# Kernel optimization log

Hardware: AMD Instinct MI355X
Metric: run time of the kernel (lower is better)

## Reference

```python
import jax, jax.numpy as jnp
import numpy as np

# Window-batch of 16x16 windows from a U-Net stage
B, C, H, W = 128, 128, 16, 16
HEADS = 8
EQK, EV = 128, 512      # embed_dim_qk, embed_dim_v (embed_dim=512, ratio=4)
L = H * W               # tokens per window (stride=1)


def _conv3x3(x, w, b):
    # NCHW 3x3 conv, padding 1
    out = jax.lax.conv_general_dilated(x, w, (1, 1), ((1, 1), (1, 1)),
                                       dimension_numbers=('NCHW', 'OIHW', 'NCHW'))
    return out + b[None, :, None, None]


def _pos_att(q, wq, bq, wk, bk, wv, bv, wo, bo, gamma):
    # MultiHeadAttention2D_POS, stride=1 -> conv_q/k/v are 1x1 convs
    hd, hdv = EQK // HEADS, EV // HEADS

    def proj(x, w, bias, d):
        y = jnp.einsum('bchw,ec->behw', x, w) + bias[None, :, None, None]
        return y.reshape(B, HEADS, d, L).transpose(0, 1, 3, 2)  # (B,h,L,d)

    pq = proj(q, wq, bq, hd)
    pk = proj(q, wk, bk, hd)
    pv = proj(q, wv, bv, hdv)
    attn = jax.nn.softmax(jnp.einsum('bhqd,bhkd->bhqk', pq, pk) * hd ** -0.5, axis=-1)
    out = jnp.einsum('bhqk,bhkd->bhqd', attn, pv)
    out = out.transpose(0, 1, 3, 2).reshape(B, EV, H, W)
    out = _conv3x3(out, wo, bo)             # proj_out: 3x3 conv EV->C
    return q + out * gamma                  # gamma-scaled residual


def _cha_att(q, wq, bq, wk, bk, wv, bv, wo, bo, gamma):
    # MultiHeadAttention2D_CHA: depthwise 1x1 grouped convs (channel multiplier = HEADS),
    # attention over the CHANNEL axis. Faithfully reproduces torch's reshape of the
    # group-major (c*HEADS+h) channel layout into (B, heads, C, L).
    def dwproj(x, w, bias):
        y = (x[:, :, None] * w.reshape(C, HEADS)[None, :, :, None, None]
             + bias.reshape(C, HEADS)[None, :, :, None, None])
        return y.reshape(B, C * HEADS, H, W).reshape(B, HEADS, C, L)

    pq = dwproj(q, wq, bq)
    pk = dwproj(q, wk, bk)
    pv = dwproj(q, wv, bv)
    attn = jax.nn.softmax(jnp.einsum('bhcl,bhdl->bhcd', pq, pk) * L ** -0.5, axis=-1)
    out = jnp.einsum('bhcd,bhdl->bhcl', attn, pv)      # (B,h,C,L)
    out = out.reshape(B, HEADS * C, H, W)
    # proj_out: grouped 1x1 ConvTranspose (== grouped 1x1 conv): sum each HEADS-sized group
    out = (out.reshape(B, C, HEADS, H, W)
           * wo.reshape(C, HEADS)[None, :, :, None, None]).sum(2) + bo[None, :, None, None]
    return q + out * gamma


def _forward(qkv_pos, qkv_cha,
             pos_wq, pos_bq, pos_wk, pos_bk, pos_wv, pos_bv, pos_wo, pos_bo, gamma_pos,
             cha_wq, cha_bq, cha_wk, cha_bk, cha_wv, cha_bv, cha_wo, cha_bo, gamma_cha,
             fuse_w, fuse_b):
    out_pos = _pos_att(qkv_pos, pos_wq, pos_bq, pos_wk, pos_bk, pos_wv, pos_bv,
                       pos_wo, pos_bo, gamma_pos)
    out_cha = _cha_att(qkv_cha, cha_wq, cha_bq, cha_wk, cha_bk, cha_wv, cha_bv,
                       cha_wo, cha_bo, gamma_cha)
    out = (out_pos + out_cha) * 0.5          # att_fusion='add' (slides=0 -> full slices)
    return _conv3x3(out, fuse_w, fuse_b)     # conv_out (Dropout2d is identity at eval)


def setup_inputs() -> dict:
    key = jax.random.key(0)
    ks = jax.random.split(key, 24)
    n = lambda k, shape, s=0.05: jax.random.normal(k, shape, dtype=jnp.float32) * s
    return {
        'qkv_pos': jax.random.normal(ks[0], (B, C, H, W), jnp.float32),
        'qkv_cha': jax.random.normal(ks[1], (B, C, H, W), jnp.float32),
        'pos_wq': n(ks[2], (EQK, C)), 'pos_bq': n(ks[3], (EQK,)),
        'pos_wk': n(ks[4], (EQK, C)), 'pos_bk': n(ks[5], (EQK,)),
        'pos_wv': n(ks[6], (EV, C)), 'pos_bv': n(ks[7], (EV,)),
        'pos_wo': n(ks[8], (C, EV, 3, 3)), 'pos_bo': n(ks[9], (C,)),
        'gamma_pos': jnp.array(0.1, jnp.float32),
        'cha_wq': n(ks[10], (C * HEADS,)), 'cha_bq': n(ks[11], (C * HEADS,)),
        'cha_wk': n(ks[12], (C * HEADS,)), 'cha_bk': n(ks[13], (C * HEADS,)),
        'cha_wv': n(ks[14], (C * HEADS,)), 'cha_bv': n(ks[15], (C * HEADS,)),
        'cha_wo': n(ks[16], (C * HEADS,)), 'cha_bo': n(ks[17], (C,)),
        'gamma_cha': jnp.array(0.1, jnp.float32),
        'fuse_w': n(ks[18], (C, C, 3, 3)), 'fuse_b': n(ks[19], (C,)),
    }


def reference(qkv_pos, qkv_cha,
              pos_wq, pos_bq, pos_wk, pos_bk, pos_wv, pos_bv, pos_wo, pos_bo, gamma_pos,
              cha_wq, cha_bq, cha_wk, cha_bk, cha_wv, cha_bv, cha_wo, cha_bo, gamma_cha,
              fuse_w, fuse_b):
    return _forward(qkv_pos, qkv_cha,
                    pos_wq, pos_bq, pos_wk, pos_bk, pos_wv, pos_bv, pos_wo, pos_bo, gamma_pos,
                    cha_wq, cha_bq, cha_wk, cha_bk, cha_wv, cha_bv, cha_wo, cha_bo, gamma_cha,
                    fuse_w, fuse_b)
```

## Files before the change

### kernel.cpp

```cpp
#include <hip/hip_runtime.h>
#include <cstdint>
#include <cstddef>

typedef unsigned short ushort_t;
typedef unsigned int uint_t;
typedef __attribute__((ext_vector_type(8))) short bf16x8;
typedef __attribute__((ext_vector_type(4))) float f32x4;

#define NB 128
#define NC 128
#define NL 256
#define NH 8
#define HD 16
#define HDV 64
#define NEV 512
#define PHALF 4194304

__device__ __forceinline__ ushort_t f2bf(float f) {
    uint_t u = __float_as_uint(f);
    u += 0x7fffu + ((u >> 16) & 1u);
    return (ushort_t)(u >> 16);
}
__device__ __forceinline__ float bf2f(ushort_t s) {
    return __uint_as_float(((uint_t)s) << 16);
}
__device__ __forceinline__ uint_t pack2(float lo, float hi) {
    uint_t r;
    asm("v_cvt_pk_bf16_f32 %0, %1, %2" : "=v"(r) : "v"(lo), "v"(hi));
    return r;
}

template<int CIN>
__global__ __launch_bounds__(256) void k_wpack(const float* __restrict__ w,
                                               short* __restrict__ wp) {
    int idx = blockIdx.x * 256 + threadIdx.x;
    if (idx >= CIN * 1152) return;
    int j    = idx & 7;
    int lane = (idx >> 3) & 63;
    int frag = idx >> 9;
    int rt   = frag & 7;
    int tap  = (frag >> 3) % 9;
    int ch   = frag / 72;
    int co   = rt * 16 + (lane & 15);
    int g    = lane >> 4;
    int ci   = ch * 32 + g * 8 + j;
    wp[idx] = (short)f2bf(w[((size_t)co * CIN + ci) * 9 + tap]);
}

template<int E>
__global__ __launch_bounds__(256) void k_wpack_qkv(const float* __restrict__ w,
                                                   short* __restrict__ wp) {
    int idx = blockIdx.x * 256 + threadIdx.x;
    if (idx >= E * 128) return;
    int j    = idx & 7;
    int lane = (idx >> 3) & 63;
    int ch   = (idx >> 9) & 3;
    int rt   = idx >> 11;
    int n = lane & 15, g = lane >> 4;
    wp[idx] = (short)f2bf(w[(size_t)(rt*16 + n)*128 + ch*32 + g*8 + j]);
}

__global__ __launch_bounds__(256) void k_xpose(const float* __restrict__ x,
                                               ushort_t* __restrict__ xbf) {
    const int half = blockIdx.x, b = blockIdx.y, t = threadIdx.x;
    const float* src = x + (size_t)b*NC*NL + (size_t)half*64*NL + t;
    uint_t* dst = (uint_t*)(xbf + ((size_t)b*NL + t)*NC + half*64);
    #pragma unroll
    for (int k8 = 0; k8 < 8; ++k8) {
        uint4 u;
        u.x = pack2(src[(k8*8+0)*NL], src[(k8*8+1)*NL]);
        u.y = pack2(src[(k8*8+2)*NL], src[(k8*8+3)*NL]);
        u.z = pack2(src[(k8*8+4)*NL], src[(k8*8+5)*NL]);
        u.w = pack2(src[(k8*8+6)*NL], src[(k8*8+7)*NL]);
        *(uint4*)(dst + k8*4) = u;
    }
}

__global__ __launch_bounds__(256) void k_pos_mfma(
    const ushort_t* __restrict__ xbf,
    const short* __restrict__ wpq, const short* __restrict__ wpk,
    const short* __restrict__ wpv,
    const float* __restrict__ bq, const float* __restrict__ bk,
    const float* __restrict__ bv,
    ushort_t* __restrict__ att)
{
    const int h = blockIdx.x, b = blockIdx.y;
    const int t = threadIdx.x;
    const int lane = t & 63, w = t >> 6;
    const int n = lane & 15, g = lane >> 4;

    __shared__ __align__(16) short lds[31744];

    const f32x4 z4 = {0.f, 0.f, 0.f, 0.f};
    f32x4 qacc[4], kacc[4], vacc[4][4];
    #pragma unroll
    for (int ct = 0; ct < 4; ++ct) { qacc[ct] = z4; kacc[ct] = z4; }
    #pragma unroll
    for (int vt = 0; vt < 4; ++vt)
        #pragma unroll
        for (int ct = 0; ct < 4; ++ct) vacc[vt][ct] = z4;

    const ushort_t* xr = xbf + ((size_t)(b*NL + w*64 + n))*NC;

    #pragma unroll 2
    for (int ch = 0; ch < 4; ++ch) {
        bf16x8 xb[4];
        #pragma unroll
        for (int ct = 0; ct < 4; ++ct)
            xb[ct] = *(const bf16x8*)(xr + ct*16*NC + ch*32 + g*8);
        const size_t fo = ((size_t)((h*4 + ch)*64) + lane) * 8;
        {
            bf16x8 aq = *(const bf16x8*)(wpq + fo);
            #pragma unroll
            for (int ct = 0; ct < 4; ++ct)
                qacc[ct] = __builtin_amdgcn_mfma_f32_16x16x32_bf16(aq, xb[ct], qacc[ct], 0, 0, 0);
        }
        {
            bf16x8 ak = *(const bf16x8*)(wpk + fo);
            #pragma unroll
            for (int ct = 0; ct < 4; ++ct)
                kacc[ct] = __builtin_amdgcn_mfma_f32_16x16x32_bf16(ak, xb[ct], kacc[ct], 0, 0, 0);
        }
        #pragma unroll
        for (int vt = 0; vt < 4; ++vt) {
            bf16x8 av = *(const bf16x8*)(wpv + ((size_t)((((h*4 + vt)*4) + ch)*64) + lane) * 8);
            #pragma unroll
            for (int ct = 0; ct < 4; ++ct)
                vacc[vt][ct] = __builtin_amdgcn_mfma_f32_16x16x32_bf16(xb[ct], av, vacc[vt][ct], 0, 0, 0);
        }
    }

    {
        float bqv[4], bkv[4];
        #pragma unroll
        for (int r = 0; r < 4; ++r) {
            bqv[r] = bq[h*16 + g*4 + r];
            bkv[r] = bk[h*16 + g*4 + r];
        }
        #pragma unroll
        for (int ct = 0; ct < 4; ++ct) {
            uint2 qp, kp;
            qp.x = pack2(qacc[ct][0] + bqv[0], qacc[ct][1] + bqv[1]);
            qp.y = pack2(qacc[ct][2] + bqv[2], qacc[ct][3] + bqv[3]);
            *(uint2*)&lds[6144 + w*1536 + (ct*16 + n)*24 + g*4] = qp;
            kp.x = pack2(kacc[ct][0] + bkv[0], kacc[ct][1] + bkv[1]);
            kp.y = pack2(kacc[ct][2] + bkv[2], kacc[ct][3] + bkv[3]);
            *(uint2*)&lds[(w*64 + ct*16 + n)*24 + g*4] = kp;
        }
        #pragma unroll
        for (int vt = 0; vt < 4; ++vt) {
            const float bvv = bv[h*64 + vt*16 + n];
            #pragma unroll
            for (int ct = 0; ct < 4; ++ct) {
                uint2 vp;
                vp.x = pack2(vacc[vt][ct][0] + bvv, vacc[vt][ct][1] + bvv);
                vp.y = pack2(vacc[vt][ct][2] + bvv, vacc[vt][ct][3] + bvv);
                *(uint2*)&lds[14848 + (vt*16 + n)*264 + w*64 + ct*16 + g*4] = vp;
            }
        }
    }
    __syncthreads();

    #pragma unroll 1
    for (int qt = 0; qt < 4; ++qt) {
        bf16x8 qf = (bf16x8){0,0,0,0,0,0,0,0};
        if (g < 2) qf = *(const bf16x8*)&lds[6144 + w*1536 + (qt*16 + n)*24 + g*8];
        f32x4 s[16];
        #pragma unroll
        for (int kt = 0; kt < 16; ++kt) {
            bf16x8 kf = (bf16x8){0,0,0,0,0,0,0,0};
            if (g < 2) kf = *(const bf16x8*)&lds[(kt*16 + n)*24 + g*8];
            s[kt] = __builtin_amdgcn_mfma_f32_16x16x32_bf16(kf, qf, z4, 0, 0, 0);
        }
        float den = 0.f;
        #pragma unroll
        for (int kt = 0; kt < 16; ++kt)
            #pragma unroll
            for (int r = 0; r < 4; ++r) {
                float e = exp2f(s[kt][r] * 0.36067376022224085f);
                s[kt][r] = e;
                den += e;
            }
        den += __shfl_xor(den, 16);
        den += __shfl_xor(den, 32);
        const float inv = 1.f / den;

        f32x4 oacc[4] = {z4, z4, z4, z4};
        #pragma unroll
        for (int c2 = 0; c2 < 8; ++c2) {
            #pragma unroll
            for (int u = 0; u < 2; ++u) {
                const int kt = 2*c2 + u;
                uint2 pp;
                pp.x = pack2(s[kt][0], s[kt][1]);
                pp.y = pack2(s[kt][2], s[kt][3]);
                *(uint2*)&lds[12288 + w*640 + n*40 + u*16 + g*4] = pp;
            }
            bf16x8 pf = *(const bf16x8*)&lds[12288 + w*640 + n*40 + g*8];
            #pragma unroll
            for (int vt = 0; vt < 4; ++vt) {
                bf16x8 av = *(const bf16x8*)&lds[14848 + (vt*16 + n)*264 + c2*32 + g*8];
                oacc[vt] = __builtin_amdgcn_mfma_f32_16x16x32_bf16(av, pf, oacc[vt], 0, 0, 0);
            }
        }
        ushort_t* ap = att + (((size_t)b*NL + (w*64 + qt*16 + n))*NEV + h*HDV + g*4);
        #pragma unroll
        for (int vt = 0; vt < 4; ++vt) {
            uint2 op;
            op.x = pack2(oacc[vt][0]*inv, oacc[vt][1]*inv);
            op.y = pack2(oacc[vt][2]*inv, oacc[vt][3]*inv);
            *(uint2*)(ap + vt*16) = op;
        }
    }
}

__global__ __launch_bounds__(512, 2) void k_conv_ci(
    const ushort_t* __restrict__ att, const short* __restrict__ wp,
    ushort_t* __restrict__ P)
{
    const int kc = blockIdx.x, b = blockIdx.y;
    const int t = threadIdx.x;
    const int lane = t & 63, w = t >> 6;
    const int wr = w >> 2, wc = w & 3;
    const int n = lane & 15, gl = lane >> 4;

    __shared__ __align__(16) short ims[2][10368];

    {
        bf16x8 z = {0,0,0,0,0,0,0,0};
        bf16x8* p = (bf16x8*)&ims[0][0];
        for (int i = t; i < 2592; i += 512) p[i] = z;
    }

    f32x4 acc[4][4];
    #pragma unroll
    for (int i = 0; i < 4; ++i)
        #pragma unroll
        for (int j = 0; j < 4; ++j) acc[i][j] = (f32x4){0.f,0.f,0.f,0.f};

    const int g1 = t & 3, x1 = (t >> 2) & 15, y1 = t >> 6;
    const ushort_t* src1 = att + ((size_t)(b*NL + y1*16 + x1))*NEV + kc*256 + g1*8;
    const ushort_t* src2 = att + ((size_t)(b*NL + (y1+8)*16 + x1))*NEV + kc*256 + g1*8;
    const int slot1 = (((y1+1)*4 + g1)*18 + x1 + 1) * 8;
    const int slot2 = (((y1+9)*4 + g1)*18 + x1 + 1) * 8;

    bf16x8 v1 = *(const bf16x8*)src1;
    bf16x8 v2 = *(const bf16x8*)src2;
    __syncthreads();

    #pragma unroll 1
    for (int ch = 0; ch < 8; ++ch) {
        short* buf = &ims[ch & 1][0];
        *(bf16x8*)&buf[slot1] = v1;
        *(bf16x8*)&buf[slot2] = v2;
        if (ch < 7) {
            v1 = *(const bf16x8*)(src1 + (ch + 1) * 32);
            v2 = *(const bf16x8*)(src2 + (ch + 1) * 32);
        }
        __syncthreads();
        #pragma unroll
        for (int tap = 0; tap < 9; ++tap) {
            const int dy = tap / 3, dx = tap % 3;
            bf16x8 Bf[4];
            #pragma unroll
            for (int ct = 0; ct < 4; ++ct)
                Bf[ct] = *(const bf16x8*)&buf[((((wc*4 + ct + dy)*4) + gl)*18 + n + dx) * 8];
            bf16x8 Af[4];
            #pragma unroll
            for (int rt = 0; rt < 4; ++rt)
                Af[rt] = *(const bf16x8*)(wp +
                    ((size_t)(((kc*8 + ch)*9 + tap)*8 + wr*4 + rt)) * 512 + lane*8);
            #pragma unroll
            for (int rt = 0; rt < 4; ++rt)
                #pragma unroll
                for (int ct = 0; ct < 4; ++ct)
                    acc[rt][ct] = __builtin_amdgcn_mfma_f32_16x16x32_bf16(
                        Af[rt], Bf[ct], acc[rt][ct], 0, 0, 0);
        }
    }

    ushort_t* Pb = P + (size_t)kc * PHALF + (size_t)b * NL * NC;
    #pragma unroll
    for (int rt = 0; rt < 4; ++rt) {
        const int co0 = wr*64 + rt*16 + gl*4;
        #pragma unroll
        for (int ct = 0; ct < 4; ++ct) {
            const int l = wc*64 + ct*16 + n;
            uint2 u;
            u.x = pack2(acc[rt][ct][0], acc[rt][ct][1]);
            u.y = pack2(acc[rt][ct][2], acc[rt][ct][3]);
            *(uint2*)(Pb + (size_t)l*NC + co0) = u;
        }
    }
}

__global__ __launch_bounds__(512, 2) void k_conv_co(
    const float* __restrict__ comb, const short* __restrict__ wp,
    const float* __restrict__ bias, float* __restrict__ out)
{
    const int kc = blockIdx.x, b = blockIdx.y;
    const int t = threadIdx.x;
    const int lane = t & 63, w = t >> 6;
    const int wr = w & 1, wc = w >> 1;
    const int n = lane & 15, gl = lane >> 4;

    __shared__ __align__(16) short ims[2][10368];

    {
        bf16x8 z = {0,0,0,0,0,0,0,0};
        bf16x8* p = (bf16x8*)&ims[0][0];
        for (int i = t; i < 2592; i += 512) p[i] = z;
    }

    f32x4 acc[2][4];
    #pragma unroll
    for (int i = 0; i < 2; ++i)
        #pragma unroll
        for (int j = 0; j < 4; ++j) acc[i][j] = (f32x4){0.f,0.f,0.f,0.f};

    const int g1 = t & 3, x1 = (t >> 2) & 15, y1 = t >> 6;
    const float* s1 = comb + ((size_t)(b*NL + y1*16 + x1))*NC + g1*8;
    const float* s2 = comb + ((size_t)(b*NL + (y1+8)*16 + x1))*NC + g1*8;
    const int slot1 = (((y1+1)*4 + g1)*18 + x1 + 1) * 8;
    const int slot2 = (((y1+9)*4 + g1)*18 + x1 + 1) * 8;

    float4 a1 = *(const float4*)s1,       b1_ = *(const float4*)(s1 + 4);
    float4 a2 = *(const float4*)s2,       b2_ = *(const float4*)(s2 + 4);
    __syncthreads();

    #pragma unroll 1
    for (int ch = 0; ch < 4; ++ch) {
        short* buf = &ims[ch & 1][0];
        uint4 w1, w2;
        w1.x = pack2(a1.x, a1.y);   w1.y = pack2(a1.z, a1.w);
        w1.z = pack2(b1_.x, b1_.y); w1.w = pack2(b1_.z, b1_.w);
        w2.x = pack2(a2.x, a2.y);   w2.y = pack2(a2.z, a2.w);
        w2.z = pack2(b2_.x, b2_.y); w2.w = pack2(b2_.z, b2_.w);
        *(uint4*)&buf[slot1] = w1;
        *(uint4*)&buf[slot2] = w2;
        if (ch < 3) {
            a1  = *(const float4*)(s1 + (ch+1)*32);
            b1_ = *(const float4*)(s1 + (ch+1)*32 + 4);
            a2  = *(const float4*)(s2 + (ch+1)*32);
            b2_ = *(const float4*)(s2 + (ch+1)*32 + 4);
        }
        __syncthreads();
        #pragma unroll
        for (int tap = 0; tap < 9; ++tap) {
            const int dy = tap / 3, dx = tap % 3;
            bf16x8 Bf[4];
            #pragma unroll
            for (int ct = 0; ct < 4; ++ct)
                Bf[ct] = *(const bf16x8*)&buf[((((wc*4 + ct + dy)*4) + gl)*18 + n + dx) * 8];
            bf16x8 Af[2];
            #pragma unroll
            for (int rt = 0; rt < 2; ++rt)
                Af[rt] = *(const bf16x8*)(wp +
                    ((size_t)((ch*9 + tap)*8 + kc*4 + wr*2 + rt)) * 512 + lane*8);
            #pragma unroll
            for (int rt = 0; rt < 2; ++rt)
                #pragma unroll
                for (int ct = 0; ct < 4; ++ct)
                    acc[rt][ct] = __builtin_amdgcn_mfma_f32_16x16x32_bf16(
                        Af[rt], Bf[ct], acc[rt][ct], 0, 0, 0);
        }
    }

    #pragma unroll
    for (int rt = 0; rt < 2; ++rt) {
        const int co0 = kc*64 + wr*32 + rt*16 + gl*4;
        const float c0 = bias[co0+0], c1 = bias[co0+1],
                    c2 = bias[co0+2], c3 = bias[co0+3];
        #pragma unroll
        for (int ct = 0; ct < 4; ++ct) {
            const int l = wc*64 + ct*16 + n;
            f32x4 a = acc[rt][ct];
            out[((size_t)b*NC + co0+0)*NL + l] = c0 + a[0];
            out[((size_t)b*NC + co0+1)*NL + l] = c1 + a[1];
            out[((size_t)b*NC + co0+2)*NL + l] = c2 + a[2];
            out[((size_t)b*NC + co0+3)*NL + l] = c3 + a[3];
        }
    }
}

#define NLP 260
__global__ __launch_bounds__(256) void k_cha(
    const float* __restrict__ xc,
    const float* __restrict__ cwq, const float* __restrict__ cbq,
    const float* __restrict__ cwk, const float* __restrict__ cbk,
    const float* __restrict__ cwv, const float* __restrict__ cbv,
    const float* __restrict__ cwo, const float* __restrict__ cbo,
    const float* __restrict__ gamma,
    const ushort_t* __restrict__ P, const float* __restrict__ qpos,
    const float* __restrict__ pbo, const float* __restrict__ gpos,
    float* __restrict__ comb)
{
    const int h = blockIdx.x, b = blockIdx.y, t = threadIdx.x;
    __shared__ float qh[16][NLP];
    __shared__ float G_s[16][17];
    __shared__ float S_s[16];
    __shared__ float wq_s[128], bq_s[128], wk_s[128], bk_s[128], wv_s[128], bv_s[128];
    __shared__ float A_s[128][17];
    __shared__ float B_s[128];
    __shared__ float M_s[16][17];
    __shared__ float c_s[16];

    #pragma unroll
    for (int j = 0; j < 16; ++j)
        qh[j][t] = xc[((size_t)b*NC + h*16 + j)*NL + t];
    if (t < 128) {
        const int k = h*128 + t;
        wq_s[t] = cwq[k]; bq_s[t] = cbq[k];
        wk_s[t] = cwk[k]; bk_s[t] = cbk[k];
        wv_s[t] = cwv[k]; bv_s[t] = cbv[k];
    }
    __syncthreads();
    {
        const int i = t >> 4, j = t & 15;
        const float4* qi = (const float4*)qh[i];
        const float4* qj = (const float4*)qh[j];
        float gg = 0.f;
        for (int l4 = 0; l4 < NL/4; ++l4) {
            float4 a = qi[l4], c = qj[l4];
            gg = fmaf(a.x,c.x,fmaf(a.y,c.y,fmaf(a.z,c.z,fmaf(a.w,c.w,gg))));
        }
        G_s[i][j] = gg;
    }
    if (t < 16) {
        const float4* qi = (const float4*)qh[t];
        float s = 0.f;
        for (int l4 = 0; l4 < NL/4; ++l4) { float4 a = qi[l4]; s += a.x + a.y + a.z + a.w; }
        S_s[t] = s;
    }
    __syncthreads();
    if (t < 128) {
        const int c2 = t, cg = c2 >> 3;
        const float wqc = wq_s[c2], bqc = bq_s[c2];
        float Pv[16];
        #pragma unroll
        for (int j = 0; j < 16; ++j) Pv[j] = wqc*G_s[cg][j] + bqc*S_s[j];
        const float Qc = wqc*S_s[cg] + bqc*256.0f;
        float mx = -3.0e38f;
        #pragma unroll
        for (int dg = 0; dg < 16; ++dg) {
            #pragma unroll
            for (int dj = 0; dj < 8; ++dj) {
                const int d = dg*8 + dj;
                float s = wk_s[d]*Pv[dg] + bk_s[d]*Qc;
                mx = fmaxf(mx, s);
            }
        }
        float A[16];
        #pragma unroll
        for (int j = 0; j < 16; ++j) A[j] = 0.f;
        float Bv = 0.f, den = 0.f;
        #pragma unroll
        for (int dg = 0; dg < 16; ++dg) {
            #pragma unroll
            for (int dj = 0; dj < 8; ++dj) {
                const int d = dg*8 + dj;
                float s = wk_s[d]*Pv[dg] + bk_s[d]*Qc;
                float e = __expf((s - mx) * 0.0625f);
                den += e;
                A[dg] = fmaf(e, wv_s[d], A[dg]);
                Bv = fmaf(e, bv_s[d], Bv);
            }
        }
        const float inv = 1.f / den;
        #pragma unroll
        for (int j = 0; j < 16; ++j) A_s[c2][j] = A[j]*inv;
        B_s[c2] = Bv*inv;
    }
    __syncthreads();
    {
        const int cl = t >> 4, j = t & 15;
        const int cp = h*16 + cl;
        float m = 0.f;
        #pragma unroll
        for (int hp = 0; hp < 8; ++hp)
            m = fmaf(cwo[cp*8+hp], A_s[cl*8+hp][j], m);
        M_s[cl][j] = m;
        if (j == 0) {
            float cc = cbo[cp];
            #pragma unroll
            for (int hp = 0; hp < 8; ++hp)
                cc = fmaf(cwo[cp*8+hp], B_s[cl*8+hp], cc);
            c_s[cl] = cc;
        }
    }
    __syncthreads();
    {
        const float g  = gamma[0];
        const float gp = gpos[0];
        const int l = t;
        float av[16];
        #pragma unroll
        for (int cl = 0; cl < 16; ++cl) {
            float a = c_s[cl];
            #pragma unroll
            for (int j = 0; j < 16; ++j)
                a = fmaf(M_s[cl][j], qh[j][l], a);
            av[cl] = a;
        }
        const ushort_t* p0 = P + ((size_t)b*NL + l)*NC + h*16;
        const ushort_t* p1 = p0 + PHALF;
        const float* qp = qpos + ((size_t)b*NC + h*16)*NL + l;
        float4* cp4 = (float4*)(comb + ((size_t)b*NL + l)*NC + h*16);
        #pragma unroll
        for (int q = 0; q < 4; ++q) {
            uint2 u0 = *(const uint2*)(p0 + 4*q);
            uint2 u1 = *(const uint2*)(p1 + 4*q);
            float s0 = bf2f((ushort_t)(u0.x & 0xffffu)) + bf2f((ushort_t)(u1.x & 0xffffu));
            float s1 = bf2f((ushort_t)(u0.x >> 16))     + bf2f((ushort_t)(u1.x >> 16));
            float s2 = bf2f((ushort_t)(u0.y & 0xffffu)) + bf2f((ushort_t)(u1.y & 0xffffu));
            float s3 = bf2f((ushort_t)(u0.y >> 16))     + bf2f((ushort_t)(u1.y >> 16));
            float4 c;
            c.x = 0.5f*(qp[(4*q+0)*NL] + gp*(pbo[h*16+4*q+0] + s0) + qh[4*q+0][l] + g*av[4*q+0]);
            c.y = 0.5f*(qp[(4*q+1)*NL] + gp*(pbo[h*16+4*q+1] + s1) + qh[4*q+1][l] + g*av[4*q+1]);
            c.z = 0.5f*(qp[(4*q+2)*NL] + gp*(pbo[h*16+4*q+2] + s2) + qh[4*q+2][l] + g*av[4*q+2]);
            c.w = 0.5f*(qp[(4*q+3)*NL] + gp*(pbo[h*16+4*q+3] + s3) + qh[4*q+3][l] + g*av[4*q+3]);
            cp4[q] = c;
        }
    }
}

extern "C" void kernel_launch(void* const* d_in, const int* in_sizes, int n_in,
                              void* d_out, int out_size, void* d_ws, size_t ws_size,
                              hipStream_t stream)
{
    const float* qpos = (const float*)d_in[0];
    const float* qcha = (const float*)d_in[1];
    const float* pwq  = (const float*)d_in[2];
    const float* pbq  = (const float*)d_in[3];
    const float* pwk  = (const float*)d_in[4];
    const float* pbk  = (const float*)d_in[5];
    const float* pwv  = (const float*)d_in[6];
    const float* pbv  = (const float*)d_in[7];
    const float* pwo  = (const float*)d_in[8];
    const float* pbo  = (const float*)d_in[9];
    const float* gpos = (const float*)d_in[10];
    const float* cwq  = (const float*)d_in[11];
    const float* cbq  = (const float*)d_in[12];
    const float* cwk  = (const float*)d_in[13];
    const float* cbk  = (const float*)d_in[14];
    const float* cwv  = (const float*)d_in[15];
    const float* cbv  = (const float*)d_in[16];
    const float* cwo  = (const float*)d_in[17];
    const float* cbo  = (const float*)d_in[18];
    const float* gcha = (const float*)d_in[19];
    const float* fw   = (const float*)d_in[20];
    const float* fb   = (const float*)d_in[21];
    float* outp = (float*)d_out;

    char* ws = (char*)d_ws;
    ushort_t* att  = (ushort_t*)ws;
    float*    comb = (float*)ws;
    ushort_t* P    = (ushort_t*)(ws + 33554432);
    ushort_t* xbf  = (ushort_t*)(ws + 33554432);
    short*    wp1  = (short*)(ws + 50331648);
    short*    wp2  = (short*)(ws + 51511296);
    short*    wpq  = (short*)(ws + 51806208);
    short*    wpk  = (short*)(ws + 51838976);
    short*    wpv  = (short*)(ws + 51871744);

    k_wpack<NEV><<<dim3((NEV*1152 + 255)/256), 256, 0, stream>>>(pwo, wp1);
    k_wpack<NC ><<<dim3((NC *1152 + 255)/256), 256, 0, stream>>>(fw,  wp2);
    k_wpack_qkv<128><<<dim3(64),  256, 0, stream>>>(pwq, wpq);
    k_wpack_qkv<128><<<dim3(64),  256, 0, stream>>>(pwk, wpk);
    k_wpack_qkv<512><<<dim3(256), 256, 0, stream>>>(pwv, wpv);

    k_xpose<<<dim3(2, NB), 256, 0, stream>>>(qpos, xbf);
    k_pos_mfma<<<dim3(NH, NB), 256, 0, stream>>>(xbf, wpq, wpk, wpv,
                                                 pbq, pbk, pbv, att);
    k_conv_ci<<<dim3(2, NB), 512, 0, stream>>>(att, wp1, P);
    k_cha<<<dim3(NH, NB), 256, 0, stream>>>(qcha, cwq, cbq, cwk, cbk, cwv, cbv,
                                            cwo, cbo, gcha,
                                            P, qpos, pbo, gpos, comb);
    k_conv_co<<<dim3(2, NB), 512, 0, stream>>>(comb, wp2, fb, outp);
}
```

Baseline: 181.8 us.

## Shrink attention LDS via bpermute Q exchange and split conv_ci by row halves

New measurement: 181.6 us. About the same (-0.1%).

```diff
diff --git a/kernel.cpp b/kernel.cpp
--- a/kernel.cpp
+++ b/kernel.cpp
@@ -89,7 +89,7 @@
     const int lane = t & 63, w = t >> 6;
     const int n = lane & 15, g = lane >> 4;
 
-    __shared__ __align__(16) short lds[31744];
+    __shared__ __align__(16) short lds[23552];
 
     const f32x4 z4 = {0.f, 0.f, 0.f, 0.f};
     f32x4 qacc[4], kacc[4], vacc[4][4];
@@ -130,6 +130,7 @@
         }
     }
 
+    uint_t qu01[4], qu23[4];
     {
         float bqv[4], bkv[4];
         #pragma unroll
@@ -139,13 +140,12 @@
         }
         #pragma unroll
         for (int ct = 0; ct < 4; ++ct) {
-            uint2 qp, kp;
-            qp.x = pack2(qacc[ct][0] + bqv[0], qacc[ct][1] + bqv[1]);
-            qp.y = pack2(qacc[ct][2] + bqv[2], qacc[ct][3] + bqv[3]);
-            *(uint2*)&lds[6144 + w*1536 + (ct*16 + n)*24 + g*4] = qp;
+            qu01[ct] = pack2(qacc[ct][0] + bqv[0], qacc[ct][1] + bqv[1]);
+            qu23[ct] = pack2(qacc[ct][2] + bqv[2], qacc[ct][3] + bqv[3]);
+            uint2 kp;
             kp.x = pack2(kacc[ct][0] + bkv[0], kacc[ct][1] + bkv[1]);
             kp.y = pack2(kacc[ct][2] + bkv[2], kacc[ct][3] + bkv[3]);
-            *(uint2*)&lds[(w*64 + ct*16 + n)*24 + g*4] = kp;
+            *(uint2*)&lds[(w*64 + ct*16 + n)*16 + g*4] = kp;
         }
         #pragma unroll
         for (int vt = 0; vt < 4; ++vt) {
@@ -155,21 +155,28 @@
                 uint2 vp;
                 vp.x = pack2(vacc[vt][ct][0] + bvv, vacc[vt][ct][1] + bvv);
                 vp.y = pack2(vacc[vt][ct][2] + bvv, vacc[vt][ct][3] + bvv);
-                *(uint2*)&lds[14848 + (vt*16 + n)*264 + w*64 + ct*16 + g*4] = vp;
+                *(uint2*)&lds[6656 + (vt*16 + n)*264 + w*64 + ct*16 + g*4] = vp;
             }
         }
     }
     __syncthreads();
 
+    const int a0 = (n + 32*(g & 1)) * 4;
     #pragma unroll 1
     for (int qt = 0; qt < 4; ++qt) {
-        bf16x8 qf = (bf16x8){0,0,0,0,0,0,0,0};
-        if (g < 2) qf = *(const bf16x8*)&lds[6144 + w*1536 + (qt*16 + n)*24 + g*8];
+        union { uint_t u[4]; bf16x8 v; } qfu;
+        qfu.u[0] = (uint_t)__builtin_amdgcn_ds_bpermute(a0,      (int)qu01[qt]);
+        qfu.u[1] = (uint_t)__builtin_amdgcn_ds_bpermute(a0,      (int)qu23[qt]);
+        qfu.u[2] = (uint_t)__builtin_amdgcn_ds_bpermute(a0 + 64, (int)qu01[qt]);
+        qfu.u[3] = (uint_t)__builtin_amdgcn_ds_bpermute(a0 + 64, (int)qu23[qt]);
+        if (g >= 2) { qfu.u[0] = 0; qfu.u[1] = 0; qfu.u[2] = 0; qfu.u[3] = 0; }
+        bf16x8 qf = qfu.v;
+
         f32x4 s[16];
         #pragma unroll
         for (int kt = 0; kt < 16; ++kt) {
             bf16x8 kf = (bf16x8){0,0,0,0,0,0,0,0};
-            if (g < 2) kf = *(const bf16x8*)&lds[(kt*16 + n)*24 + g*8];
+            if (g < 2) kf = *(const bf16x8*)&lds[(kt*16 + n)*16 + g*8];
             s[kt] = __builtin_amdgcn_mfma_f32_16x16x32_bf16(kf, qf, z4, 0, 0, 0);
         }
         float den = 0.f;
@@ -194,12 +201,12 @@
                 uint2 pp;
                 pp.x = pack2(s[kt][0], s[kt][1]);
                 pp.y = pack2(s[kt][2], s[kt][3]);
-                *(uint2*)&lds[12288 + w*640 + n*40 + u*16 + g*4] = pp;
+                *(uint2*)&lds[4096 + w*640 + n*40 + u*16 + g*4] = pp;
             }
-            bf16x8 pf = *(const bf16x8*)&lds[12288 + w*640 + n*40 + g*8];
+            bf16x8 pf = *(const bf16x8*)&lds[4096 + w*640 + n*40 + g*8];
             #pragma unroll
             for (int vt = 0; vt < 4; ++vt) {
-                bf16x8 av = *(const bf16x8*)&lds[14848 + (vt*16 + n)*264 + c2*32 + g*8];
+                bf16x8 av = *(const bf16x8*)&lds[6656 + (vt*16 + n)*264 + c2*32 + g*8];
                 oacc[vt] = __builtin_amdgcn_mfma_f32_16x16x32_bf16(av, pf, oacc[vt], 0, 0, 0);
             }
         }
@@ -214,22 +221,23 @@
     }
 }
 
-__global__ __launch_bounds__(512, 2) void k_conv_ci(
+__global__ __launch_bounds__(256, 3) void k_conv_ci(
     const ushort_t* __restrict__ att, const short* __restrict__ wp,
     ushort_t* __restrict__ P)
 {
-    const int kc = blockIdx.x, b = blockIdx.y;
+    const int kc = blockIdx.x >> 1, lh = blockIdx.x & 1, b = blockIdx.y;
     const int t = threadIdx.x;
     const int lane = t & 63, w = t >> 6;
-    const int wr = w >> 2, wc = w & 3;
+    const int wr = w >> 1, wc = w & 1;
     const int n = lane & 15, gl = lane >> 4;
-
-    __shared__ __align__(16) short ims[2][10368];
+    const int y0 = lh * 8;
+
+    __shared__ __align__(16) short ims[2][5760];
 
     {
         bf16x8 z = {0,0,0,0,0,0,0,0};
         bf16x8* p = (bf16x8*)&ims[0][0];
-        for (int i = t; i < 2592; i += 512) p[i] = z;
+        for (int i = t; i < 1440; i += 256) p[i] = z;
     }
 
     f32x4 acc[4][4];
@@ -238,14 +246,27 @@
         #pragma unroll
         for (int j = 0; j < 4; ++j) acc[i][j] = (f32x4){0.f,0.f,0.f,0.f};
 
-    const int g1 = t & 3, x1 = (t >> 2) & 15, y1 = t >> 6;
-    const ushort_t* src1 = att + ((size_t)(b*NL + y1*16 + x1))*NEV + kc*256 + g1*8;
-    const ushort_t* src2 = att + ((size_t)(b*NL + (y1+8)*16 + x1))*NEV + kc*256 + g1*8;
-    const int slot1 = (((y1+1)*4 + g1)*18 + x1 + 1) * 8;
-    const int slot2 = (((y1+9)*4 + g1)*18 + x1 + 1) * 8;
-
-    bf16x8 v1 = *(const bf16x8*)src1;
-    bf16x8 v2 = *(const bf16x8*)src2;
+    const int gg1 = t & 3,        xx1 = (t >> 2) & 15,        yp1 = t >> 6;
+    const int id2 = t + 256;
+    const int gg2 = id2 & 3,      xx2 = (id2 >> 2) & 15,      yp2 = id2 >> 6;
+    const int id3 = t + 512;
+    const int gg3 = id3 & 3,      xx3 = (id3 >> 2) & 15,      yp3 = id3 >> 6;
+    const bool has3 = (t < 128);
+    const int y1 = y0 - 1 + yp1, y2 = y0 - 1 + yp2, y3 = y0 - 1 + yp3;
+    const bool ok1 = (y1 >= 0) && (y1 < 16);
+    const bool ok2 = (y2 >= 0) && (y2 < 16);
+    const bool ok3 = has3 && (y3 >= 0) && (y3 < 16);
+    const ushort_t* src1 = att + ((size_t)(b*NL + y1*16 + xx1))*NEV + kc*256 + gg1*8;
+    const ushort_t* src2 = att + ((size_t)(b*NL + y2*16 + xx2))*NEV + kc*256 + gg2*8;
+    const ushort_t* src3 = att + ((size_t)(b*NL + y3*16 + xx3))*NEV + kc*256 + gg3*8;
+    const int slot1 = ((yp1*4 + gg1)*18 + xx1 + 1) * 8;
+    const int slot2 = ((yp2*4 + gg2)*18 + xx2 + 1) * 8;
+    const int slot3 = ((yp3*4 + gg3)*18 + xx3 + 1) * 8;
+
+    bf16x8 v1 = {0,0,0,0,0,0,0,0}, v2 = v1, v3 = v1;
+    if (ok1) v1 = *(const bf16x8*)src1;
+    if (ok2) v2 = *(const bf16x8*)src2;
+    if (ok3) v3 = *(const bf16x8*)src3;
     __syncthreads();
 
     #pragma unroll 1
@@ -253,9 +274,11 @@
         short* buf = &ims[ch & 1][0];
         *(bf16x8*)&buf[slot1] = v1;
         *(bf16x8*)&buf[slot2] = v2;
+        if (has3) *(bf16x8*)&buf[slot3] = v3;
         if (ch < 7) {
-            v1 = *(const bf16x8*)(src1 + (ch + 1) * 32);
-            v2 = *(const bf16x8*)(src2 + (ch + 1) * 32);
+            if (ok1) v1 = *(const bf16x8*)(src1 + (ch + 1) * 32);
+            if (ok2) v2 = *(const bf16x8*)(src2 + (ch + 1) * 32);
+            if (ok3) v3 = *(const bf16x8*)(src3 + (ch + 1) * 32);
         }
         __syncthreads();
         #pragma unroll
@@ -264,7 +287,7 @@
             bf16x8 Bf[4];
             #pragma unroll
             for (int ct = 0; ct < 4; ++ct)
-                Bf[ct] = *(const bf16x8*)&buf[((((wc*4 + ct + dy)*4) + gl)*18 + n + dx) * 8];
+                Bf[ct] = *(const bf16x8*)&buf[(((wc*4 + ct + dy)*4 + gl)*18 + n + dx) * 8];
             bf16x8 Af[4];
             #pragma unroll
             for (int rt = 0; rt < 4; ++rt)
@@ -285,7 +308,7 @@
         const int co0 = wr*64 + rt*16 + gl*4;
         #pragma unroll
         for (int ct = 0; ct < 4; ++ct) {
-            const int l = wc*64 + ct*16 + n;
+            const int l = lh*128 + wc*64 + ct*16 + n;
             uint2 u;
             u.x = pack2(acc[rt][ct][0], acc[rt][ct][1]);
             u.y = pack2(acc[rt][ct][2], acc[rt][ct][3]);
@@ -572,7 +595,7 @@
     k_xpose<<<dim3(2, NB), 256, 0, stream>>>(qpos, xbf);
     k_pos_mfma<<<dim3(NH, NB), 256, 0, stream>>>(xbf, wpq, wpk, wpv,
                                                  pbq, pbk, pbv, att);
-    k_conv_ci<<<dim3(2, NB), 512, 0, stream>>>(att, wp1, P);
+    k_conv_ci<<<dim3(4, NB), 256, 0, stream>>>(att, wp1, P);
     k_cha<<<dim3(NH, NB), 256, 0, stream>>>(qcha, cwq, cbq, cwk, cbk, cwv, cbv,
                                             cwo, cbo, gcha,
                                             P, qpos, pbo, gpos, comb);
```
